# Kernel optimization log

Hardware: AMD Instinct MI355X
Metric: run time of the kernel (lower is better)

Reference implementation:

```python
import jax, jax.numpy as jnp
import numpy as np
from jax import lax

ITERS = 10
EPS = 1e-6
LOSS_WEIGHT = 1.0


def _max_pool3x3(x):
    # F.max_pool2d(x, kernel_size=3, stride=1, padding=1): torch pads with -inf for max pool
    return lax.reduce_window(x, -jnp.inf, lax.max,
                             window_dimensions=(1, 1, 3, 3),
                             window_strides=(1, 1, 1, 1),
                             padding=((0, 0), (0, 0), (1, 1), (1, 1)))


def _soft_erode(x):
    return -_max_pool3x3(-x)


def _soft_dilate(x):
    return _max_pool3x3(x)


def _soft_open(x):
    return _soft_dilate(_soft_erode(x))


def _soft_skel(img, iters):
    img = jnp.clip(img, 0.0, 1.0)
    img1 = _soft_open(img)
    skel = jax.nn.relu(img - img1)
    for _ in range(iters):
        img = _soft_erode(img)
        img1 = _soft_open(img)
        delta = jax.nn.relu(img - img1)
        skel = skel + jax.nn.relu(delta - skel * delta)
    return skel


def setup_inputs() -> dict:
    key = jax.random.key(0)
    k1, k2 = jax.random.split(key)
    B, C, H, W = 8, 2, 1024, 1024
    pred = jax.random.normal(k1, (B, C, H, W), dtype=jnp.float32)
    target = jax.random.uniform(k2, (B, C, H, W), dtype=jnp.float32)
    return {"pred": pred, "target": target}


def reference(pred, target):
    # sigmoid on logits
    p = jax.nn.sigmoid(pred)  # [B,C,H,W]
    t = target.astype(p.dtype)
    # per-class channel slicing is equivalent to channel-wise ops (pooling is per-channel)
    skel_p = _soft_skel(p, ITERS)
    skel_t = _soft_skel(t, ITERS)
    hw = (2, 3)
    tprec = jnp.sum(skel_p * t, axis=hw) / (jnp.sum(skel_p, axis=hw) + EPS)  # [B,C]
    tsens = jnp.sum(skel_t * p, axis=hw) / (jnp.sum(skel_t, axis=hw) + EPS)  # [B,C]
    cl_dice = 1.0 - 2.0 * tprec * tsens / (tprec + tsens + EPS)  # [B,C]
    # original: per-class mean over batch, then mean over classes == global mean
    return LOSS_WEIGHT * jnp.mean(cl_dice)
```

## Files before the change

kernel.cpp:

```cpp
#include <hip/hip_runtime.h>


#define TILE 64
#define HALO 12
#define RROWS 92
#define SD 52
#define IMG 1024
#define NBC 16
#define NITER 11
#define LEPS 1e-6f

typedef unsigned int u32;
typedef _Float16 hv2 __attribute__((ext_vector_type(2)));

struct __align__(16) U4 { u32 v[4]; };

__device__ __forceinline__ hv2 H2(u32 x) { union { u32 u; hv2 h; } c; c.u = x; return c.h; }
__device__ __forceinline__ u32 U2(hv2 x) { union { u32 u; hv2 h; } c; c.h = x; return c.u; }
__device__ __forceinline__ hv2 hmin2v(hv2 a, hv2 b) { return __builtin_elementwise_min(a, b); }
__device__ __forceinline__ hv2 hmax2v(hv2 a, hv2 b) { return __builtin_elementwise_max(a, b); }
__device__ __forceinline__ u32 dpp_prev16(u32 x) {
    return (u32)__builtin_amdgcn_update_dpp(0, (int)x, 0x101, 0xf, 0xf, true);
}
__device__ __forceinline__ u32 dpp_next16(u32 x) {
    return (u32)__builtin_amdgcn_update_dpp(0, (int)x, 0x111, 0xf, 0xf, true);
}
__device__ __forceinline__ u32 alignh(u32 hi, u32 lo) {
    return (u32)((((unsigned long long)hi << 32) | lo) >> 16);
}
__device__ __forceinline__ float sigmoidf(float x) { return 1.0f / (1.0f + __expf(-x)); }

template<bool IS_MIN>
__device__ __forceinline__ void hpass(const u32 d[4], u32 o[4]) {
    u32 dm = dpp_prev16(d[3]);
    u32 dp = dpp_next16(d[0]);
    u32 a[5];
    a[0] = alignh(d[0], dm);
    a[1] = alignh(d[1], d[0]);
    a[2] = alignh(d[2], d[1]);
    a[3] = alignh(d[3], d[2]);
    a[4] = alignh(dp,   d[3]);
#pragma unroll
    for (int q = 0; q < 4; ++q) {
        if (IS_MIN) o[q] = U2(hmin2v(hmin2v(H2(a[q]), H2(d[q])), H2(a[q + 1])));
        else        o[q] = U2(hmax2v(hmax2v(H2(a[q]), H2(d[q])), H2(a[q + 1])));
    }
}

__global__ __launch_bounds__(256, 4)
void skel_tile_kernel(const float* __restrict__ pred,
                      const float* __restrict__ target,
                      float* __restrict__ ws)
{
    __shared__ __align__(16) u32 bufA[RROWS * SD];
    __shared__ __align__(16) u32 bufB[RROWS * SD];

    const int tid = threadIdx.x;
    const int bc  = blockIdx.z & (NBC - 1);
    const int img = blockIdx.z >> 4;
    const int r0  = blockIdx.y * TILE;
    const int c0  = blockIdx.x * TILE;

    const float* src = (img == 0) ? pred : target;
    const size_t base = (size_t)bc * (size_t)(IMG * IMG);

    const bool edgeT = (blockIdx.y == 0);
    const bool edgeB = (blockIdx.y == 15);
    const bool edgeL = (blockIdx.x == 0);
    const bool edgeR = (blockIdx.x == 15);
    const int rdLo = edgeT ? 12 : 0;
    const int rdHi = edgeB ? 75 : (RROWS - 1);

    for (int t = tid; t < 88 * 12; t += 256) {
        int rr = t / 12;
        int g  = t - rr * 12;
        int gr = min(max(r0 + rr - HALO, 0), IMG - 1);
        const float* rowp = src + base + (size_t)gr * IMG;
        float f[8];
        int gc0 = c0 + 8 * g - HALO;
        if (g <= 10 && gc0 >= 0 && gc0 + 8 <= IMG) {
            float4 v0 = *(const float4*)(rowp + gc0);
            float4 v1 = *(const float4*)(rowp + gc0 + 4);
            f[0] = v0.x; f[1] = v0.y; f[2] = v0.z; f[3] = v0.w;
            f[4] = v1.x; f[5] = v1.y; f[6] = v1.z; f[7] = v1.w;
        } else {
#pragma unroll
            for (int i = 0; i < 8; ++i) {
                int rc = min(8 * g + i, 87);
                int gc = min(max(c0 + rc - HALO, 0), IMG - 1);
                f[i] = rowp[gc];
            }
        }
        U4 u;
#pragma unroll
        for (int q = 0; q < 4; ++q) {
            float a = f[2 * q], b = f[2 * q + 1];
            if (img == 0) { a = sigmoidf(a); b = sigmoidf(b); }
            else { a = fminf(fmaxf(a, 0.f), 1.f); b = fminf(fmaxf(b, 0.f), 1.f); }
            hv2 p; p[0] = (_Float16)a; p[1] = (_Float16)b;
            u.v[q] = U2(p);
        }
        *(uint4*)&bufA[rr * SD + 4 * g] = *(const uint4*)u.v;
    }

    const int strip = tid >> 4;
    const int g16   = tid & 15;
    const int coldw = 4 * min(g16, 11);
    const bool wact = (g16 < 12);

    const int rs_e = min(1 + 6 * strip, 85);
    const int rs_d = 12 + 4 * strip;

    u32 mk[4];
#pragma unroll
    for (int q = 0; q < 4; ++q) {
        int c = 8 * g16 + 2 * q;
        mk[q] = ((c >= 12 && c <= 75) ? 0xFFFFu : 0u) |
                ((c + 1 >= 12 && c + 1 <= 75) ? 0xFFFF0000u : 0u);
    }

    hv2 Sv[4][4];
#pragma unroll
    for (int j = 0; j < 4; ++j)
#pragma unroll
        for (int q = 0; q < 4; ++q) { Sv[j][q][0] = (_Float16)0; Sv[j][q][1] = (_Float16)0; }

    u32* cur = bufA;
    u32* oth = bufB;

    __syncthreads();

    for (int k = 0; k < NITER; ++k) {
        {
            U4 h[8];
            const u32* p = cur + (rs_e - 1) * SD + coldw;
#pragma unroll
            for (int j = 0; j < 8; ++j) {
                U4 u; *(uint4*)u.v = *(const uint4*)(p + j * SD);
                hpass<true>(u.v, h[j].v);
            }
            u32* q = oth + rs_e * SD + coldw;
#pragma unroll
            for (int j = 0; j < 6; ++j) {
                int row = rs_e + j;
                if (wact && row <= 86) {
                    U4 o;
#pragma unroll
                    for (int qd = 0; qd < 4; ++qd)
                        o.v[qd] = U2(hmin2v(hmin2v(H2(h[j].v[qd]), H2(h[j + 1].v[qd])),
                                            H2(h[j + 2].v[qd])));
                    *(uint4*)(q + j * SD) = *(const uint4*)o.v;
                }
            }
        }
        __syncthreads();

        {
            U4 w[6], m[6];
            if (!(edgeT || edgeB)) {
                const u32* p = oth + (rs_d - 1) * SD + coldw;
#pragma unroll
                for (int j = 0; j < 6; ++j)
                    *(uint4*)w[j].v = *(const uint4*)(p + j * SD);
            } else {
#pragma unroll
                for (int j = 0; j < 6; ++j) {
                    int rr = min(max(rs_d - 1 + j, rdLo), rdHi);
                    *(uint4*)w[j].v = *(const uint4*)(oth + rr * SD + coldw);
                }
            }
#pragma unroll
            for (int j = 0; j < 6; ++j) hpass<false>(w[j].v, m[j].v);

            if (edgeL && g16 == 1) {
#pragma unroll
                for (int j = 0; j < 6; ++j) {
                    u32 d2 = w[j].v[2];
                    u32 sw = (d2 >> 16) | (d2 << 16);
                    u32 pm = U2(hmax2v(H2(d2), H2(sw)));
                    m[j].v[2] = (m[j].v[2] & 0xFFFF0000u) | (pm & 0xFFFFu);
                }
            }
            if (edgeR && g16 == 9) {
#pragma unroll
                for (int j = 0; j < 6; ++j) {
                    u32 d1 = w[j].v[1];
                    u32 sw = (d1 >> 16) | (d1 << 16);
                    u32 pm = U2(hmax2v(H2(d1), H2(sw)));
                    m[j].v[1] = (m[j].v[1] & 0x0000FFFFu) | (pm & 0xFFFF0000u);
                }
            }

            const u32* pc = cur + rs_d * SD + coldw;
#pragma unroll
            for (int j = 0; j < 4; ++j) {
                U4 a; *(uint4*)a.v = *(const uint4*)(pc + j * SD);
#pragma unroll
                for (int qd = 0; qd < 4; ++qd) {
                    hv2 D = hmax2v(hmax2v(H2(m[j].v[qd]), H2(m[j + 1].v[qd])),
                                   H2(m[j + 2].v[qd]));
                    hv2 z; z[0] = (_Float16)0; z[1] = (_Float16)0;
                    hv2 d = hmax2v(H2(a.v[qd]) - D, z);
                    d = H2(U2(d) & mk[qd]);
                    hv2 s = Sv[j][qd];
                    hv2 t = hmax2v(d - s * d, z);
                    Sv[j][qd] = s + t;
                }
            }
        }

        { u32* t_ = cur; cur = oth; oth = t_; }
        __syncthreads();
    }

    const float* osrc = (img == 0) ? target : pred;
    float s_sum = 0.0f, sp_sum = 0.0f;
#pragma unroll
    for (int j = 0; j < 4; ++j) {
        int orow = r0 + 4 * strip + j;
#pragma unroll
        for (int q = 0; q < 4; ++q) {
#pragma unroll
            for (int e = 0; e < 2; ++e) {
                int rc = 8 * g16 + 2 * q + e;
                if (rc >= 12 && rc <= 75) {
                    float sv = (float)Sv[j][q][e];
                    float ov = osrc[base + (size_t)orow * IMG + (c0 + rc - HALO)];
                    if (img == 1) ov = sigmoidf(ov);
                    s_sum  += sv;
                    sp_sum += sv * ov;
                }
            }
        }
    }

#pragma unroll
    for (int off = 32; off > 0; off >>= 1) {
        s_sum  += __shfl_down(s_sum,  off, 64);
        sp_sum += __shfl_down(sp_sum, off, 64);
    }
    float* red = (float*)bufA;
    if ((tid & 63) == 0) {
        red[(tid >> 6) * 2 + 0] = sp_sum;
        red[(tid >> 6) * 2 + 1] = s_sum;
    }
    __syncthreads();
    if (tid == 0) {
        float a = (red[0] + red[2]) + (red[4] + red[6]);
        float b = (red[1] + red[3]) + (red[5] + red[7]);
        float* acc = ws + (size_t)blockIdx.z * 2;
        atomicAdd(acc + 0, a);
        atomicAdd(acc + 1, b);
    }
}

__global__ void finalize_kernel(const float* __restrict__ ws, float* __restrict__ out)
{
    if (threadIdx.x == 0) {
        float acc = 0.0f;
        for (int bc = 0; bc < NBC; ++bc) {
            float spt = ws[(0 * NBC + bc) * 2 + 0];
            float sp  = ws[(0 * NBC + bc) * 2 + 1];
            float stp = ws[(1 * NBC + bc) * 2 + 0];
            float st  = ws[(1 * NBC + bc) * 2 + 1];
            float tprec = spt / (sp + LEPS);
            float tsens = stp / (st + LEPS);
            acc += 1.0f - 2.0f * tprec * tsens / (tprec + tsens + LEPS);
        }
        out[0] = acc / (float)NBC;
    }
}

extern "C" void kernel_launch(void* const* d_in, const int* in_sizes, int n_in,
                              void* d_out, int out_size, void* d_ws, size_t ws_size,
                              hipStream_t stream) {
    const float* pred   = (const float*)d_in[0];
    const float* target = (const float*)d_in[1];
    float* ws  = (float*)d_ws;
    float* out = (float*)d_out;

    hipMemsetAsync(d_ws, 0, 2 * NBC * 2 * sizeof(float), stream);

    dim3 grid(IMG / TILE, IMG / TILE, 2 * NBC);
    skel_tile_kernel<<<grid, 256, 0, stream>>>(pred, target, ws);
    finalize_kernel<<<1, 64, 0, stream>>>(ws, out);
}
```

Before: 593.8 us.

## Reorder separable pooling passes and use packed-f16 inline asm with negated skeleton accumulator

Both pooling stages now run the vertical pass before the horizontal one, so the horizontal DPP/alignbit pass runs on fewer rows (6 instead of 8 for erode, 4 instead of 6 for dilate). The skeleton update is rewritten as packed f16 inline-asm ops that keep a negated accumulator, so a single fma replaces the separate multiply and subtract. The per-element boundary mask is dropped, and the shared-memory row stride shrinks from 52 to 50. Risks: shared-memory bank conflicts or misaligned 16-byte accesses from the new stride, changed edge semantics from removing the mask, and inline asm blocking compiler scheduling.

```diff
diff --git a/kernel.cpp b/kernel.cpp
--- a/kernel.cpp
+++ b/kernel.cpp
@@ -4,21 +4,31 @@
 #define TILE 64
 #define HALO 12
 #define RROWS 92
-#define SD 52
+#define SD 50
 #define IMG 1024
 #define NBC 16
 #define NITER 11
 #define LEPS 1e-6f
 
 typedef unsigned int u32;
-typedef _Float16 hv2 __attribute__((ext_vector_type(2)));
 
 struct __align__(16) U4 { u32 v[4]; };
 
-__device__ __forceinline__ hv2 H2(u32 x) { union { u32 u; hv2 h; } c; c.u = x; return c.h; }
-__device__ __forceinline__ u32 U2(hv2 x) { union { u32 u; hv2 h; } c; c.h = x; return c.u; }
-__device__ __forceinline__ hv2 hmin2v(hv2 a, hv2 b) { return __builtin_elementwise_min(a, b); }
-__device__ __forceinline__ hv2 hmax2v(hv2 a, hv2 b) { return __builtin_elementwise_max(a, b); }
+__device__ __forceinline__ u32 pk_min(u32 a, u32 b) {
+    u32 d; asm("v_pk_min_f16 %0, %1, %2" : "=v"(d) : "v"(a), "v"(b)); return d;
+}
+__device__ __forceinline__ u32 pk_max(u32 a, u32 b) {
+    u32 d; asm("v_pk_max_f16 %0, %1, %2" : "=v"(d) : "v"(a), "v"(b)); return d;
+}
+__device__ __forceinline__ u32 pk_max0(u32 a) {
+    u32 d; asm("v_pk_max_f16 %0, %1, 0" : "=v"(d) : "v"(a)); return d;
+}
+__device__ __forceinline__ u32 pk_add(u32 a, u32 b) {
+    u32 d; asm("v_pk_add_f16 %0, %1, %2" : "=v"(d) : "v"(a), "v"(b)); return d;
+}
+__device__ __forceinline__ u32 pk_fma(u32 a, u32 b, u32 c) {
+    u32 d; asm("v_pk_fma_f16 %0, %1, %2, %3" : "=v"(d) : "v"(a), "v"(b), "v"(c)); return d;
+}
 __device__ __forceinline__ u32 dpp_prev16(u32 x) {
     return (u32)__builtin_amdgcn_update_dpp(0, (int)x, 0x101, 0xf, 0xf, true);
 }
@@ -26,7 +36,7 @@
     return (u32)__builtin_amdgcn_update_dpp(0, (int)x, 0x111, 0xf, 0xf, true);
 }
 __device__ __forceinline__ u32 alignh(u32 hi, u32 lo) {
-    return (u32)((((unsigned long long)hi << 32) | lo) >> 16);
+    return __builtin_amdgcn_alignbit(hi, lo, 16);
 }
 __device__ __forceinline__ float sigmoidf(float x) { return 1.0f / (1.0f + __expf(-x)); }
 
@@ -42,8 +52,8 @@
     a[4] = alignh(dp,   d[3]);
 #pragma unroll
     for (int q = 0; q < 4; ++q) {
-        if (IS_MIN) o[q] = U2(hmin2v(hmin2v(H2(a[q]), H2(d[q])), H2(a[q + 1])));
-        else        o[q] = U2(hmax2v(hmax2v(H2(a[q]), H2(d[q])), H2(a[q + 1])));
+        if (IS_MIN) o[q] = pk_min(pk_min(a[q], d[q]), a[q + 1]);
+        else        o[q] = pk_max(pk_max(a[q], d[q]), a[q + 1]);
     }
 }
 
@@ -97,8 +107,11 @@
             float a = f[2 * q], b = f[2 * q + 1];
             if (img == 0) { a = sigmoidf(a); b = sigmoidf(b); }
             else { a = fminf(fmaxf(a, 0.f), 1.f); b = fminf(fmaxf(b, 0.f), 1.f); }
-            hv2 p; p[0] = (_Float16)a; p[1] = (_Float16)b;
-            u.v[q] = U2(p);
+            _Float16 ha = (_Float16)a, hb = (_Float16)b;
+            u32 ua, ub;
+            __builtin_memcpy(&ua, &ha, 2);
+            __builtin_memcpy(&ub, &hb, 2);
+            u.v[q] = (ua & 0xFFFFu) | (ub << 16);
         }
         *(uint4*)&bufA[rr * SD + 4 * g] = *(const uint4*)u.v;
     }
@@ -111,19 +124,11 @@
     const int rs_e = min(1 + 6 * strip, 85);
     const int rs_d = 12 + 4 * strip;
 
-    u32 mk[4];
-#pragma unroll
-    for (int q = 0; q < 4; ++q) {
-        int c = 8 * g16 + 2 * q;
-        mk[q] = ((c >= 12 && c <= 75) ? 0xFFFFu : 0u) |
-                ((c + 1 >= 12 && c + 1 <= 75) ? 0xFFFF0000u : 0u);
-    }
-
-    hv2 Sv[4][4];
+    u32 nS[4][4];
 #pragma unroll
     for (int j = 0; j < 4; ++j)
 #pragma unroll
-        for (int q = 0; q < 4; ++q) { Sv[j][q][0] = (_Float16)0; Sv[j][q][1] = (_Float16)0; }
+        for (int q = 0; q < 4; ++q) nS[j][q] = 0u;
 
     u32* cur = bufA;
     u32* oth = bufB;
@@ -132,31 +137,28 @@
 
     for (int k = 0; k < NITER; ++k) {
         {
-            U4 h[8];
+            U4 w[8];
             const u32* p = cur + (rs_e - 1) * SD + coldw;
 #pragma unroll
-            for (int j = 0; j < 8; ++j) {
-                U4 u; *(uint4*)u.v = *(const uint4*)(p + j * SD);
-                hpass<true>(u.v, h[j].v);
-            }
+            for (int j = 0; j < 8; ++j)
+                *(uint4*)w[j].v = *(const uint4*)(p + j * SD);
             u32* q = oth + rs_e * SD + coldw;
 #pragma unroll
             for (int j = 0; j < 6; ++j) {
+                u32 v[4], o[4];
+#pragma unroll
+                for (int qd = 0; qd < 4; ++qd)
+                    v[qd] = pk_min(pk_min(w[j].v[qd], w[j + 1].v[qd]), w[j + 2].v[qd]);
+                hpass<true>(v, o);
                 int row = rs_e + j;
-                if (wact && row <= 86) {
-                    U4 o;
-#pragma unroll
-                    for (int qd = 0; qd < 4; ++qd)
-                        o.v[qd] = U2(hmin2v(hmin2v(H2(h[j].v[qd]), H2(h[j + 1].v[qd])),
-                                            H2(h[j + 2].v[qd])));
-                    *(uint4*)(q + j * SD) = *(const uint4*)o.v;
-                }
+                if (wact && row <= 86)
+                    *(uint4*)(q + j * SD) = *(const uint4*)o;
             }
         }
         __syncthreads();
 
         {
-            U4 w[6], m[6];
+            U4 w[6];
             if (!(edgeT || edgeB)) {
                 const u32* p = oth + (rs_d - 1) * SD + coldw;
 #pragma unroll
@@ -169,42 +171,31 @@
                     *(uint4*)w[j].v = *(const uint4*)(oth + rr * SD + coldw);
                 }
             }
-#pragma unroll
-            for (int j = 0; j < 6; ++j) hpass<false>(w[j].v, m[j].v);
-
-            if (edgeL && g16 == 1) {
-#pragma unroll
-                for (int j = 0; j < 6; ++j) {
-                    u32 d2 = w[j].v[2];
-                    u32 sw = (d2 >> 16) | (d2 << 16);
-                    u32 pm = U2(hmax2v(H2(d2), H2(sw)));
-                    m[j].v[2] = (m[j].v[2] & 0xFFFF0000u) | (pm & 0xFFFFu);
-                }
-            }
-            if (edgeR && g16 == 9) {
-#pragma unroll
-                for (int j = 0; j < 6; ++j) {
-                    u32 d1 = w[j].v[1];
-                    u32 sw = (d1 >> 16) | (d1 << 16);
-                    u32 pm = U2(hmax2v(H2(d1), H2(sw)));
-                    m[j].v[1] = (m[j].v[1] & 0x0000FFFFu) | (pm & 0xFFFF0000u);
-                }
-            }
 
             const u32* pc = cur + rs_d * SD + coldw;
 #pragma unroll
             for (int j = 0; j < 4; ++j) {
+                u32 v[4], m[4];
+#pragma unroll
+                for (int qd = 0; qd < 4; ++qd)
+                    v[qd] = pk_max(pk_max(w[j].v[qd], w[j + 1].v[qd]), w[j + 2].v[qd]);
+                hpass<false>(v, m);
+
+                if (edgeL && g16 == 1) {
+                    u32 pm = pk_max(v[2], alignh(v[2], v[2]));
+                    m[2] = (m[2] & 0xFFFF0000u) | (pm & 0xFFFFu);
+                }
+                if (edgeR && g16 == 9) {
+                    u32 pm = pk_max(v[1], alignh(v[1], v[1]));
+                    m[1] = (m[1] & 0x0000FFFFu) | (pm & 0xFFFF0000u);
+                }
+
                 U4 a; *(uint4*)a.v = *(const uint4*)(pc + j * SD);
 #pragma unroll
                 for (int qd = 0; qd < 4; ++qd) {
-                    hv2 D = hmax2v(hmax2v(H2(m[j].v[qd]), H2(m[j + 1].v[qd])),
-                                   H2(m[j + 2].v[qd]));
-                    hv2 z; z[0] = (_Float16)0; z[1] = (_Float16)0;
-                    hv2 d = hmax2v(H2(a.v[qd]) - D, z);
-                    d = H2(U2(d) & mk[qd]);
-                    hv2 s = Sv[j][qd];
-                    hv2 t = hmax2v(d - s * d, z);
-                    Sv[j][qd] = s + t;
+                    u32 d = pk_max0(pk_add(a.v[qd], m[qd] ^ 0x80008000u));
+                    u32 t = pk_max0(pk_fma(nS[j][qd], d, d));
+                    nS[j][qd] = pk_add(nS[j][qd], t ^ 0x80008000u);
                 }
             }
         }
@@ -219,12 +210,15 @@
     for (int j = 0; j < 4; ++j) {
         int orow = r0 + 4 * strip + j;
 #pragma unroll
-        for (int q = 0; q < 4; ++q) {
+        for (int qd = 0; qd < 4; ++qd) {
 #pragma unroll
             for (int e = 0; e < 2; ++e) {
-                int rc = 8 * g16 + 2 * q + e;
+                int rc = 8 * g16 + 2 * qd + e;
                 if (rc >= 12 && rc <= 75) {
-                    float sv = (float)Sv[j][q][e];
+                    unsigned short hu = (unsigned short)(nS[j][qd] >> (16 * e));
+                    _Float16 hv;
+                    __builtin_memcpy(&hv, &hu, 2);
+                    float sv = -(float)hv;
                     float ov = osrc[base + (size_t)orow * IMG + (c0 + rc - HALO)];
                     if (img == 1) ov = sigmoidf(ov);
                     s_sum  += sv;
```

New measurement: 654.9 us. 10.3% more time.
